# Performance work log

Measured on AMD Instinct MI355X. Metric: run time of the kernel, lower is better.

The kernel has to match this reference:

```python
import jax, jax.numpy as jnp
import numpy as np
import math

EPS = 1e-5      # artanh boundary clamp (Poincare ball)
MIN_NORM = 1e-15

def _norm(x):
    return jnp.clip(jnp.linalg.norm(x, axis=-1, keepdims=True), MIN_NORM, None)

def artanh(x):
    x = jnp.clip(x, -1.0 + EPS, 1.0 - EPS)
    return 0.5 * (jnp.log1p(x) - jnp.log1p(-x))

def expmap0(u):
    # c = 1 Poincare ball: tanh(||u||) * u / ||u||
    n = _norm(u)
    return jnp.tanh(n) * u / n

def mobius_matvec(M, x):
    # geoopt: mx = x @ M^T; res = tanh(||mx||/||x|| * artanh(||x||)) * mx/||mx||
    xn = _norm(x)
    mx = x @ M.T
    mxn = _norm(mx)
    res = jnp.tanh(mxn / xn * artanh(xn)) * mx / mxn
    zero_row = jnp.all(mx == 0, axis=-1, keepdims=True)
    return jnp.where(zero_row, jnp.zeros_like(res), res)

def mobius_add(x, y):
    x2 = jnp.sum(x * x, axis=-1, keepdims=True)
    y2 = jnp.sum(y * y, axis=-1, keepdims=True)
    xy = jnp.sum(x * y, axis=-1, keepdims=True)
    num = (1.0 + 2.0 * xy + y2) * x + (1.0 - x2) * y
    den = 1.0 + 2.0 * xy + x2 * y2
    return num / jnp.clip(den, MIN_NORM, None)

def dist(x, y):
    # d(x,y) = 2 * artanh(|| (-x) mobius+ y ||); reduces the last dim
    return 2.0 * artanh(_norm(mobius_add(-x, y)))[..., 0]

def setup_inputs() -> dict:
    key = jax.random.key(0)
    k1, k2, k3, k4, k5 = jax.random.split(key, 5)
    B, S, H, D = 64, 1024, 768, 64
    bound = 1.0 / math.sqrt(D)
    sequence_output = jax.random.normal(k1, (B, S, H), dtype=jnp.float32) * 0.1
    proj = jax.random.uniform(k2, (H, D), dtype=jnp.float32, minval=-0.05, maxval=0.05)
    trans = jax.random.uniform(k3, (D, D), dtype=jnp.float32, minval=-0.05, maxval=0.05)
    pos = expmap0(jax.random.uniform(k4, (D,), dtype=jnp.float32, minval=-bound, maxval=bound))
    neg = expmap0(jax.random.uniform(k5, (D,), dtype=jnp.float32, minval=-bound, maxval=bound))
    return {"sequence_output": sequence_output, "proj": proj, "trans": trans,
            "pos": pos, "neg": neg}

def reference(sequence_output, proj, trans, pos, neg):
    t = sequence_output @ proj          # [B, S, 64]
    t = expmap0(t)
    t = mobius_matvec(trans, t)
    pos_logits = dist(neg, t).sum(-1)   # [B]
    neg_logits = dist(pos, t).sum(-1)   # [B]
    return jnp.stack((neg_logits, pos_logits), axis=-1)  # [B, 2]
```

## Files before the change

### kernel.cpp

```cpp
#include <hip/hip_runtime.h>
#include <math.h>

#define MIN_NORM 1e-15f
#define BOUND_EPS 1e-5f

typedef __attribute__((ext_vector_type(8))) short short8v;
typedef __attribute__((ext_vector_type(4))) float f32x4;

__device__ __forceinline__ unsigned short f2bf(float f) {
  unsigned int u = __float_as_uint(f);
  unsigned int r = (u + 0x7FFFu + ((u >> 16) & 1u)) >> 16;
  return (unsigned short)r;
}
__device__ __forceinline__ unsigned int pack2bf(float a, float b) {
  return (unsigned int)f2bf(a) | ((unsigned int)f2bf(b) << 16);
}

__device__ __forceinline__ float gred16(float v) {
  v += __shfl_xor(v, 1, 64);
  v += __shfl_xor(v, 2, 64);
  v += __shfl_xor(v, 4, 64);
  v += __shfl_xor(v, 8, 64);
  return v;
}
__device__ __forceinline__ float wred64(float v) {
#pragma unroll
  for (int off = 32; off; off >>= 1) v += __shfl_xor(v, off, 64);
  return v;
}
__device__ __forceinline__ float artanh_c(float x) {
  x = fminf(fmaxf(x, -1.f + BOUND_EPS), 1.f - BOUND_EPS);
  return 0.5f * logf((1.f + x) / (1.f - x));
}

__global__ __launch_bounds__(256) void poincare_prep(
    const float* __restrict__ proj, const float* __restrict__ trans,
    unsigned short* __restrict__ projB, unsigned short* __restrict__ transB) {
  int idx = blockIdx.x * 256 + threadIdx.x;
  if (idx < 49152) {
    int k = idx >> 6, d = idx & 63;
    int kt = k >> 5, t5 = k & 31, lk = t5 >> 3, j = t5 & 7;
    int nt = d >> 4, lr = d & 15;
    int l = lk * 16 + lr;
    projB[((kt * 4 + nt) * 64 + l) * 8 + j] = f2bf(proj[idx]);
  } else if (idx < 49152 + 4096) {
    int i2 = idx - 49152;
    int r = i2 >> 6, c = i2 & 63;
    int nt = r >> 4, lr = r & 15;
    int kt = c >> 5, lk = (c >> 3) & 3, j = c & 7;
    int l = lk * 16 + lr;
    transB[((kt * 4 + nt) * 64 + l) * 8 + j] = f2bf(trans[i2]);
  }
}

__global__ __launch_bounds__(256, 3) void poincare_main(
    const float* __restrict__ seq,
    const unsigned short* __restrict__ projB,
    const unsigned short* __restrict__ transB,
    const float* __restrict__ pos, const float* __restrict__ neg,
    float* __restrict__ wsPart) {
  __shared__ unsigned short As[2][64][136];
  __shared__ unsigned short teL[4][16 * 64];
  __shared__ float partial[4][2];

  const int tid = threadIdx.x;
  const int w = tid >> 6, l = tid & 63;
  const int lr = l & 15, lk = l >> 4;
  const long bIdx = blockIdx.x;
  const float* sBase = seq + bIdx * 64 * 768;

  const int rS = tid >> 5;
  const int cS = (tid & 31) * 4;

  f32x4 acc[4];
#pragma unroll
  for (int nt = 0; nt < 4; ++nt) acc[nt] = (f32x4){0.f, 0.f, 0.f, 0.f};

#pragma unroll
  for (int i = 0; i < 8; ++i) {
    int r = i * 8 + rS;
    float4 v = *(const float4*)(sBase + r * 768 + cS);
    *(uint2*)&As[0][r][cS] = make_uint2(pack2bf(v.x, v.y), pack2bf(v.z, v.w));
  }
  __syncthreads();

#pragma unroll 2
  for (int ch = 0; ch < 6; ++ch) {
    const int cur = ch & 1;

    short8v bf[4][4];
#pragma unroll
    for (int ktl = 0; ktl < 4; ++ktl) {
      const unsigned short* pb = projB + (ch * 4 + ktl) * 2048 + l * 8;
      bf[ktl][0] = *(const short8v*)(pb);
      bf[ktl][1] = *(const short8v*)(pb + 512);
      bf[ktl][2] = *(const short8v*)(pb + 1024);
      bf[ktl][3] = *(const short8v*)(pb + 1536);
    }

    float4 st[8];
    if (ch < 5) {
#pragma unroll
      for (int i = 0; i < 8; ++i) {
        int r = i * 8 + rS;
        st[i] = *(const float4*)(sBase + r * 768 + (ch + 1) * 128 + cS);
      }
    }

#pragma unroll
    for (int ktl = 0; ktl < 4; ++ktl) {
      short8v av = *(const short8v*)&As[cur][w * 16 + lr][ktl * 32 + lk * 8];
      acc[0] = __builtin_amdgcn_mfma_f32_16x16x32_bf16(av, bf[ktl][0], acc[0], 0, 0, 0);
      acc[1] = __builtin_amdgcn_mfma_f32_16x16x32_bf16(av, bf[ktl][1], acc[1], 0, 0, 0);
      acc[2] = __builtin_amdgcn_mfma_f32_16x16x32_bf16(av, bf[ktl][2], acc[2], 0, 0, 0);
      acc[3] = __builtin_amdgcn_mfma_f32_16x16x32_bf16(av, bf[ktl][3], acc[3], 0, 0, 0);
    }

    if (ch < 5) {
#pragma unroll
      for (int i = 0; i < 8; ++i) {
        int r = i * 8 + rS;
        *(uint2*)&As[cur ^ 1][r][cS] =
            make_uint2(pack2bf(st[i].x, st[i].y), pack2bf(st[i].z, st[i].w));
      }
    }
    __syncthreads();
  }

  float th[4];
#pragma unroll
  for (int i = 0; i < 4; ++i) {
    float s = acc[0][i] * acc[0][i] + acc[1][i] * acc[1][i] +
              acc[2][i] * acc[2][i] + acc[3][i] * acc[3][i];
    s = gred16(s);
    float n = fmaxf(sqrtf(s), MIN_NORM);
    float t = tanhf(n);
    th[i] = fmaxf(t, MIN_NORM);
    float sc = t / n;
#pragma unroll
    for (int nt = 0; nt < 4; ++nt) acc[nt][i] *= sc;
  }

  unsigned short* buf = teL[w];
#pragma unroll
  for (int i = 0; i < 4; ++i) {
    int row = lk * 4 + i;
    int sw = (row & 7) << 3;
#pragma unroll
    for (int nt = 0; nt < 4; ++nt) {
      int col = nt * 16 + lr;
      buf[row * 64 + (col ^ sw)] = f2bf(acc[nt][i]);
    }
  }
  __syncthreads();

  f32x4 acc2[4];
#pragma unroll
  for (int nt = 0; nt < 4; ++nt) acc2[nt] = (f32x4){0.f, 0.f, 0.f, 0.f};
  const unsigned short* pT = transB + l * 8;
#pragma unroll
  for (int kt = 0; kt < 2; ++kt) {
    short8v a2 = *(const short8v*)&buf[lr * 64 + ((kt * 32 + lk * 8) ^ ((lr & 7) << 3))];
    const unsigned short* pt = pT + kt * 2048;
    short8v c0 = *(const short8v*)(pt);
    short8v c1 = *(const short8v*)(pt + 512);
    short8v c2 = *(const short8v*)(pt + 1024);
    short8v c3 = *(const short8v*)(pt + 1536);
    acc2[0] = __builtin_amdgcn_mfma_f32_16x16x32_bf16(a2, c0, acc2[0], 0, 0, 0);
    acc2[1] = __builtin_amdgcn_mfma_f32_16x16x32_bf16(a2, c1, acc2[1], 0, 0, 0);
    acc2[2] = __builtin_amdgcn_mfma_f32_16x16x32_bf16(a2, c2, acc2[2], 0, 0, 0);
    acc2[3] = __builtin_amdgcn_mfma_f32_16x16x32_bf16(a2, c3, acc2[3], 0, 0, 0);
  }

  float xp[4], xq[4];
#pragma unroll
  for (int nt = 0; nt < 4; ++nt) {
    xp[nt] = pos[nt * 16 + lr];
    xq[nt] = neg[nt * 16 + lr];
  }
  float x2p = wred64(xp[0] * xp[0] + xp[1] * xp[1] + xp[2] * xp[2] + xp[3] * xp[3]) * 0.25f;
  float x2n = wred64(xq[0] * xq[0] + xq[1] * xq[1] + xq[2] * xq[2] + xq[3] * xq[3]) * 0.25f;

  float distP = 0.f, distN = 0.f;
#pragma unroll
  for (int i = 0; i < 4; ++i) {
    float m0 = acc2[0][i], m1 = acc2[1][i], m2 = acc2[2][i], m3 = acc2[3][i];
    float s = gred16(m0 * m0 + m1 * m1 + m2 * m2 + m3 * m3);
    float mxn = fmaxf(sqrtf(s), MIN_NORM);
    float xn = th[i];
    float rs = tanhf(mxn / xn * artanh_c(xn)) / mxn;
    float r0 = rs * m0, r1 = rs * m1, r2 = rs * m2, r3 = rs * m3;
    float y2 = gred16(r0 * r0 + r1 * r1 + r2 * r2 + r3 * r3);
    float xyP = -gred16(xp[0] * r0 + xp[1] * r1 + xp[2] * r2 + xp[3] * r3);
    float xyN = -gred16(xq[0] * r0 + xq[1] * r1 + xq[2] * r2 + xq[3] * r3);
    {
      float A = 1.f + 2.f * xyP + y2, B = 1.f - x2p;
      float inv = 1.f / fmaxf(1.f + 2.f * xyP + x2p * y2, MIN_NORM);
      float v0 = (B * r0 - A * xp[0]) * inv, v1 = (B * r1 - A * xp[1]) * inv;
      float v2 = (B * r2 - A * xp[2]) * inv, v3 = (B * r3 - A * xp[3]) * inv;
      float nv = fmaxf(sqrtf(gred16(v0 * v0 + v1 * v1 + v2 * v2 + v3 * v3)), MIN_NORM);
      distP += 2.f * artanh_c(nv);
    }
    {
      float A = 1.f + 2.f * xyN + y2, B = 1.f - x2n;
      float inv = 1.f / fmaxf(1.f + 2.f * xyN + x2n * y2, MIN_NORM);
      float v0 = (B * r0 - A * xq[0]) * inv, v1 = (B * r1 - A * xq[1]) * inv;
      float v2 = (B * r2 - A * xq[2]) * inv, v3 = (B * r3 - A * xq[3]) * inv;
      float nv = fmaxf(sqrtf(gred16(v0 * v0 + v1 * v1 + v2 * v2 + v3 * v3)), MIN_NORM);
      distN += 2.f * artanh_c(nv);
    }
  }
  float tP = wred64(distP) * 0.0625f;
  float tN = wred64(distN) * 0.0625f;
  if (l == 0) { partial[w][0] = tP; partial[w][1] = tN; }
  __syncthreads();
  if (tid == 0) {
    wsPart[0 * 1024 + bIdx] = partial[0][0] + partial[1][0] + partial[2][0] + partial[3][0];
    wsPart[1 * 1024 + bIdx] = partial[0][1] + partial[1][1] + partial[2][1] + partial[3][1];
  }
}

__global__ __launch_bounds__(128) void poincare_reduce(const float* __restrict__ wsPart,
                                                       float* __restrict__ out) {
  int t = threadIdx.x;
  int b = t >> 1, j = t & 1;
  const float4* v = (const float4*)(wsPart + j * 1024 + b * 16);
  float s = 0.f;
#pragma unroll
  for (int i = 0; i < 4; ++i) s += v[i].x + v[i].y + v[i].z + v[i].w;
  out[b * 2 + j] = s;
}

extern "C" void kernel_launch(void* const* d_in, const int* in_sizes, int n_in,
                              void* d_out, int out_size, void* d_ws, size_t ws_size,
                              hipStream_t stream) {
  const float* seq = (const float*)d_in[0];
  const float* proj = (const float*)d_in[1];
  const float* trans = (const float*)d_in[2];
  const float* pos = (const float*)d_in[3];
  const float* neg = (const float*)d_in[4];

  unsigned short* projB = (unsigned short*)d_ws;
  unsigned short* transB = projB + 49152;
  float* wsPart = (float*)((char*)d_ws + 106496);
  float* out = (float*)d_out;

  poincare_prep<<<208, 256, 0, stream>>>(proj, trans, projB, transB);
  poincare_main<<<1024, 256, 0, stream>>>(seq, projB, transB, pos, neg, wsPart);
  poincare_reduce<<<1, 128, 0, stream>>>(wsPart, out);
}
```

Baseline: 51.06 us.

## Stream activations directly into LDS with global_load_lds and convert on read

Replaces the register-staged load-then-convert path for the sequence tile with direct global-to-LDS async loads of fp32 data (global_load_lds, 16 bytes per lane), and moves the bf16 conversion to the point where MFMA fragments are read from LDS. The K chunk shrinks from 128 to 64 columns over 12 iterations so the fp32 double buffer fits, using a padded row stride of 260 floats. This removes register pressure and VGPR round trips for staging, but doubles the number of barriers and adds per-fragment conversion work. There is no explicit wait on the async LDS loads beyond the barrier, so correctness relies on the compiler inserting vmcnt waits.

```diff
diff --git a/kernel.cpp b/kernel.cpp
--- a/kernel.cpp
+++ b/kernel.cpp
@@ -12,8 +12,11 @@
   unsigned int r = (u + 0x7FFFu + ((u >> 16) & 1u)) >> 16;
   return (unsigned short)r;
 }
-__device__ __forceinline__ unsigned int pack2bf(float a, float b) {
-  return (unsigned int)f2bf(a) | ((unsigned int)f2bf(b) << 16);
+
+__device__ __forceinline__ void gll16(const float* g, float* l) {
+  __builtin_amdgcn_global_load_lds(
+      (const __attribute__((address_space(1))) void*)g,
+      (__attribute__((address_space(3))) void*)l, 16, 0, 0);
 }
 
 __device__ __forceinline__ float gred16(float v) {
@@ -59,8 +62,8 @@
     const unsigned short* __restrict__ transB,
     const float* __restrict__ pos, const float* __restrict__ neg,
     float* __restrict__ wsPart) {
-  __shared__ unsigned short As[2][64][136];
-  __shared__ unsigned short teL[4][16 * 64];
+  __shared__ float AsF[2][16 * 260];
+  __shared__ unsigned short teL[4][1024];
   __shared__ float partial[4][2];
 
   const int tid = threadIdx.x;
@@ -69,61 +72,58 @@
   const long bIdx = blockIdx.x;
   const float* sBase = seq + bIdx * 64 * 768;
 
-  const int rS = tid >> 5;
-  const int cS = (tid & 31) * 4;
+  const int segRow = l >> 4;
+  const int segCol = (l & 15) * 4;
 
   f32x4 acc[4];
 #pragma unroll
   for (int nt = 0; nt < 4; ++nt) acc[nt] = (f32x4){0.f, 0.f, 0.f, 0.f};
 
 #pragma unroll
-  for (int i = 0; i < 8; ++i) {
-    int r = i * 8 + rS;
-    float4 v = *(const float4*)(sBase + r * 768 + cS);
-    *(uint2*)&As[0][r][cS] = make_uint2(pack2bf(v.x, v.y), pack2bf(v.z, v.w));
+  for (int s = 0; s < 4; ++s) {
+    int r = w * 16 + s * 4 + segRow;
+    gll16(sBase + r * 768 + segCol, &AsF[0][(w * 4 + s) * 260]);
   }
   __syncthreads();
 
-#pragma unroll 2
-  for (int ch = 0; ch < 6; ++ch) {
+  for (int ch = 0; ch < 12; ++ch) {
     const int cur = ch & 1;
 
-    short8v bf[4][4];
-#pragma unroll
-    for (int ktl = 0; ktl < 4; ++ktl) {
-      const unsigned short* pb = projB + (ch * 4 + ktl) * 2048 + l * 8;
+    short8v bf[2][4];
+#pragma unroll
+    for (int ktl = 0; ktl < 2; ++ktl) {
+      const unsigned short* pb = projB + (ch * 2 + ktl) * 2048 + l * 8;
       bf[ktl][0] = *(const short8v*)(pb);
       bf[ktl][1] = *(const short8v*)(pb + 512);
       bf[ktl][2] = *(const short8v*)(pb + 1024);
       bf[ktl][3] = *(const short8v*)(pb + 1536);
     }
 
-    float4 st[8];
-    if (ch < 5) {
-#pragma unroll
-      for (int i = 0; i < 8; ++i) {
-        int r = i * 8 + rS;
-        st[i] = *(const float4*)(sBase + r * 768 + (ch + 1) * 128 + cS);
+    if (ch < 11) {
+#pragma unroll
+      for (int s = 0; s < 4; ++s) {
+        int r = w * 16 + s * 4 + segRow;
+        gll16(sBase + r * 768 + (ch + 1) * 64 + segCol,
+              &AsF[cur ^ 1][(w * 4 + s) * 260]);
       }
     }
 
-#pragma unroll
-    for (int ktl = 0; ktl < 4; ++ktl) {
-      short8v av = *(const short8v*)&As[cur][w * 16 + lr][ktl * 32 + lk * 8];
+    const float* fragBase = &AsF[cur][(w * 4 + (lr >> 2)) * 260 + (lr & 3) * 64];
+#pragma unroll
+    for (int ktl = 0; ktl < 2; ++ktl) {
+      float4 lo = *(const float4*)(fragBase + ktl * 32 + lk * 8);
+      float4 hi = *(const float4*)(fragBase + ktl * 32 + lk * 8 + 4);
+      short8v av;
+      av[0] = (short)f2bf(lo.x); av[1] = (short)f2bf(lo.y);
+      av[2] = (short)f2bf(lo.z); av[3] = (short)f2bf(lo.w);
+      av[4] = (short)f2bf(hi.x); av[5] = (short)f2bf(hi.y);
+      av[6] = (short)f2bf(hi.z); av[7] = (short)f2bf(hi.w);
       acc[0] = __builtin_amdgcn_mfma_f32_16x16x32_bf16(av, bf[ktl][0], acc[0], 0, 0, 0);
       acc[1] = __builtin_amdgcn_mfma_f32_16x16x32_bf16(av, bf[ktl][1], acc[1], 0, 0, 0);
       acc[2] = __builtin_amdgcn_mfma_f32_16x16x32_bf16(av, bf[ktl][2], acc[2], 0, 0, 0);
       acc[3] = __builtin_amdgcn_mfma_f32_16x16x32_bf16(av, bf[ktl][3], acc[3], 0, 0, 0);
     }
 
-    if (ch < 5) {
-#pragma unroll
-      for (int i = 0; i < 8; ++i) {
-        int r = i * 8 + rS;
-        *(uint2*)&As[cur ^ 1][r][cS] =
-            make_uint2(pack2bf(st[i].x, st[i].y), pack2bf(st[i].z, st[i].w));
-      }
-    }
     __syncthreads();
   }
 
```

After: 60.29 us. +18.1%, slower.
